# Kernel optimization log

Measured on AMD Instinct MI355X. Metric: run time of the kernel, lower is better.

The kernel has to match this reference:

```python
import jax, jax.numpy as jnp
import numpy as np

Q, N, S, A, E, H = 2048, 64, 128, 4, 128, 8
D = E // H
NEG = -1e9

def _mlp(x, w1, b1, w2, b2):
    return jax.nn.silu(x @ w1 + b1) @ w2 + b2

def _mha(x, wq, bq, wk, bk, wv, bv, wo, bo):
    # MultiHeadAttention with default activation=relu applied to q,k,v and output
    q = jax.nn.relu(x @ wq + bq)
    k = jax.nn.relu(x @ wk + bk)
    v = jax.nn.relu(x @ wv + bv)
    def split(t):
        return t.reshape(Q, N, H, D).transpose(0, 2, 1, 3)  # [Q,H,N,D]
    qh, kh, vh = split(q), split(k), split(v)
    scores = jnp.einsum('bhqd,bhkd->bhqk', qh, kh) / (D ** 0.5)
    attn = jax.nn.softmax(scores, axis=-1)
    y = jnp.einsum('bhqk,bhkd->bhqd', attn, vh).transpose(0, 2, 1, 3).reshape(Q, N, E)
    return jax.nn.relu(y @ wo + bo)

def setup_inputs():
    key = jax.random.key(0)
    ks = jax.random.split(key, 26)
    nrm = lambda k, s: jax.random.normal(k, s, jnp.float32) * 0.05
    return {
        'tasks': jax.random.normal(ks[0], (Q, N, N + 4 * S), jnp.float32),
        'constraints': jax.random.normal(ks[1], (Q, A), jnp.float32),
        'masks': jax.random.randint(ks[2], (Q, N, S), 0, 2),
        'topologicals': jax.random.randint(ks[3], (Q, N), 0, N),
        'w_init1': nrm(ks[4], (N + A, 128)), 'b_init1': jnp.zeros((128,), jnp.float32),
        'w_init2': nrm(ks[5], (128, E)), 'b_init2': jnp.zeros((E,), jnp.float32),
        'wq': nrm(ks[6], (E, E)), 'bq': jnp.zeros((E,), jnp.float32),
        'wk': nrm(ks[7], (E, E)), 'bk': jnp.zeros((E,), jnp.float32),
        'wv': nrm(ks[8], (E, E)), 'bv': jnp.zeros((E,), jnp.float32),
        'wo': nrm(ks[9], (E, E)), 'bo': jnp.zeros((E,), jnp.float32),
        'w_node1': nrm(ks[10], (E + A, 128)), 'b_node1': jnp.zeros((128,), jnp.float32),
        'w_node2': nrm(ks[11], (128, E)), 'b_node2': jnp.zeros((E,), jnp.float32),
        'w_ser1': nrm(ks[12], (A, 128)), 'b_ser1': jnp.zeros((128,), jnp.float32),
        'w_ser2': nrm(ks[13], (128, E)), 'b_ser2': jnp.zeros((E,), jnp.float32),
    }

def reference(tasks, constraints, masks, topologicals,
              w_init1, b_init1, w_init2, b_init2,
              wq, bq, wk, bk, wv, bv, wo, bo,
              w_node1, b_node1, w_node2, b_node2,
              w_ser1, b_ser1, w_ser2, b_ser2):
    cons = jnp.broadcast_to(constraints[:, None, :], (Q, N, A))
    node_emb = _mlp(jnp.concatenate([tasks[:, :, :N], cons], -1), w_init1, b_init1, w_init2, b_init2)
    nodes_emb = _mha(node_emb, wq, bq, wk, bk, wv, bv, wo, bo) + node_emb
    # original sets channel 0 to -3 then overwrites with 3; channel 2 stays 0 (kept faithfully)
    qos = jnp.zeros((Q, N, A), jnp.float32).at[:, :, 0].set(3.0).at[:, :, 1].set(1.0).at[:, :, 3].set(1.0)
    ava = jnp.ones((Q,), jnp.float32)
    tp = jnp.full((Q,), 3.0, jnp.float32)
    rel = jnp.ones((Q,), jnp.float32)
    ridx = jnp.zeros((Q, N), jnp.float32)
    rprob = jnp.zeros((Q, N), jnp.float32)
    qidx = jnp.arange(Q)
    topo_seq = topologicals[:, ::-1].T  # [N, Q]: reversed topological order, one node per step
    keys = jax.random.split(jax.random.key(1), N)

    def step(carry, xs):
        qos, ava, tp, rel, ridx, rprob = carry
        topo, k = xs
        task = tasks[qidx, topo]                 # [Q, N + 4S] per-query gathered row
        workflow = task[:, :N]
        response_time = jnp.max(workflow * qos[:, :, 0], axis=1)  # [Q]
        qos_feat = jnp.stack([response_time, ava, tp, rel], axis=-1)
        node_e = nodes_emb[qidx, topo]           # [Q, E]
        tne = _mlp(jnp.concatenate([node_e, qos_feat], -1), w_node1, b_node1, w_node2, b_node2)
        services = task[:, N:].reshape(Q, S, A)
        ser_emb = _mlp(services, w_ser1, b_ser1, w_ser2, b_ser2)
        logits = jnp.einsum('qse,qe->qs', ser_emb, tne)
        mask = masks[qidx, topo]                 # [Q, S]
        logits = jnp.where(mask == 0, NEG, logits)
        ser_prob = jax.nn.softmax(logits, axis=-1)
        ser_idx = jax.random.categorical(k, logits)  # ~ Categorical(ser_prob)
        onehot = jax.nn.one_hot(topo, N, dtype=jnp.float32)
        ridx = ridx + onehot * ser_idx[:, None].astype(jnp.float32)
        rprob = rprob + onehot * ser_prob[qidx, ser_idx][:, None]
        base = ser_idx * 4 + N
        ser_rt = task[qidx, base]
        ser_ava = task[qidx, base + 1]
        ser_tp = task[qidx, base + 2]
        ser_rel = task[qidx, base + 3]
        new_tp = jnp.minimum(ser_tp, tp)
        qos = qos.at[qidx, topo, 0].set(ser_rt + response_time)
        qos = qos.at[qidx, topo, 1].set(ser_ava * ava)
        qos = qos.at[qidx, topo, 2].set(new_tp)
        qos = qos.at[qidx, topo, 3].set(ser_rel * rel)
        return (qos, ser_ava * ava, new_tp, ser_rel * rel, ridx, rprob), None

    (qos, ava, tp, rel, ridx, rprob), _ = jax.lax.scan(
        step, (qos, ava, tp, rel, ridx, rprob), (topo_seq, keys))
    return ridx.astype(jnp.int16), rprob
```

## Files before the change

kernel.cpp:

```cpp
#include <hip/hip_runtime.h>
#include <math.h>

#define Qn 2048
#define Nn 64
#define Sn 128
#define An 4
#define En 128
#define TASKW 576
#define NEGV -1000000000.0f

__device__ __forceinline__ void threefry2x32(unsigned k0, unsigned k1,
                                             unsigned x0, unsigned x1,
                                             unsigned& o0, unsigned& o1) {
  unsigned ks2 = k0 ^ k1 ^ 0x1BD11BDAu;
  x0 += k0; x1 += k1;
#define TFR(r) { x0 += x1; x1 = (x1 << (r)) | (x1 >> (32 - (r))); x1 ^= x0; }
  TFR(13) TFR(15) TFR(26) TFR(6)
  x0 += k1;  x1 += ks2 + 1u;
  TFR(17) TFR(29) TFR(16) TFR(24)
  x0 += ks2; x1 += k0 + 2u;
  TFR(13) TFR(15) TFR(26) TFR(6)
  x0 += k0;  x1 += k1 + 3u;
  TFR(17) TFR(29) TFR(16) TFR(24)
  x0 += k1;  x1 += ks2 + 4u;
  TFR(13) TFR(15) TFR(26) TFR(6)
  x0 += ks2; x1 += k0 + 5u;
#undef TFR
  o0 = x0; o1 = x1;
}

__device__ __forceinline__ float silu_f(float x) {
  return x / (1.0f + expf(-x));
}

__device__ __forceinline__ float fexp(float x) {
  return __builtin_amdgcn_exp2f(x * 1.44269504088896f);
}
__device__ __forceinline__ float fsilu(float x) {
  const float e = __builtin_amdgcn_exp2f(x * -1.44269504088896f);
  return x * __builtin_amdgcn_rcpf(1.0f + e);
}
__device__ __forceinline__ float flog(float x) {
  return __builtin_amdgcn_logf(x) * 0.69314718055995f;
}

__global__ void setup_kernel(const float* __restrict__ w_node2,
                             const float* __restrict__ b_node2,
                             const float* __restrict__ w_ser2,
                             const float* __restrict__ b_ser2,
                             float* __restrict__ Mbuf, float* __restrict__ dvec,
                             unsigned* __restrict__ keys) {
  const int b = blockIdx.x, t = threadIdx.x;
  if (b < 128) {
    float acc = 0.0f;
    for (int e = 0; e < 128; ++e)
      acc = fmaf(w_node2[b * 128 + e], w_ser2[t * 128 + e], acc);
    Mbuf[b * 128 + t] = acc;
  } else if (b == 128) {
    float acc = 0.0f;
    for (int e = 0; e < 128; ++e)
      acc = fmaf(b_node2[e], w_ser2[t * 128 + e], acc);
    dvec[t] = acc;
  } else {
    if (t < 64) {
      unsigned o0, o1;
      threefry2x32(0u, 1u, 0u, (unsigned)t, o0, o1);
      keys[2 * t + 0] = o0;
      keys[2 * t + 1] = o1;
    }
  }
}

__global__ __launch_bounds__(256, 2)
void init_mlp_kernel(const float* __restrict__ tasks,
                     const float* __restrict__ cons,
                     const float* __restrict__ w1, const float* __restrict__ b1,
                     const float* __restrict__ w2, const float* __restrict__ b2,
                     float* __restrict__ node_emb) {
  const int q = blockIdx.x, tid = threadIdx.x;
  const int lane = tid & 127, half = tid >> 7;
  __shared__ float xr[2][68];
  __shared__ float sgb[2][128];
  float w1r[68], w2r[128];
#pragma unroll
  for (int i = 0; i < 68; ++i) w1r[i] = w1[i * 128 + lane];
#pragma unroll
  for (int j = 0; j < 128; ++j) w2r[j] = w2[j * 128 + lane];
  const float bb1 = b1[lane], bb2 = b2[lane];
  for (int r = 0; r < 64; r += 2) {
    if (tid < 136) {
      const int rr = tid / 68, j = tid - rr * 68;
      xr[rr][j] = (j < 64) ? tasks[(q * 64 + r + rr) * TASKW + j]
                           : cons[q * 4 + (j - 64)];
    }
    __syncthreads();
    float g = 0.0f;
#pragma unroll
    for (int i = 0; i < 68; ++i) g = fmaf(xr[half][i], w1r[i], g);
    g += bb1;
    sgb[half][lane] = silu_f(g);
    __syncthreads();
    float o = 0.0f;
#pragma unroll
    for (int j = 0; j < 128; ++j) o = fmaf(sgb[half][j], w2r[j], o);
    node_emb[(q * 64 + r + half) * 128 + lane] = o + bb2;
    __syncthreads();
  }
}

__global__ __launch_bounds__(256, 2)
void mha_kernel(const float* __restrict__ node_emb,
                const float* __restrict__ wq, const float* __restrict__ bq,
                const float* __restrict__ wk, const float* __restrict__ bk,
                const float* __restrict__ wv, const float* __restrict__ bv,
                float* __restrict__ y_out) {
  const int q = blockIdx.x, tid = threadIdx.x;
  __shared__ float xs[64][130];
  __shared__ float qh[64][18];
  __shared__ float kh[64][18];
  __shared__ float vt[16][66];
  __shared__ float pool[3 * 16 * 130];
  float (*wht)[16][130] = (float (*)[16][130])pool;
  float (*at)[66] = (float (*)[66])pool;

  for (int idx = tid; idx < 64 * 128; idx += 256) {
    const int n = idx >> 7, e = idx & 127;
    xs[n][e] = node_emb[(q * 64 + n) * 128 + e];
  }
  __syncthreads();

  const int d16 = tid >> 4;
  const int ng = tid & 15;

  for (int hd = 0; hd < 8; ++hd) {
    for (int idx = tid; idx < 3 * 128 * 16; idx += 256) {
      const int m = idx >> 11, k = (idx >> 4) & 127, d = idx & 15;
      const float* W = (m == 0) ? wq : (m == 1) ? wk : wv;
      wht[m][d][k] = W[k * 128 + hd * 16 + d];
    }
    __syncthreads();

    {
      const float bqv = bq[hd * 16 + d16];
      const float bkv = bk[hd * 16 + d16];
      const float bvv = bv[hd * 16 + d16];
      const float2* wq2 = (const float2*)&wht[0][d16][0];
      const float2* wk2 = (const float2*)&wht[1][d16][0];
      const float2* wv2 = (const float2*)&wht[2][d16][0];
      const float2* xr0 = (const float2*)&xs[ng][0];
      const float2* xr1 = (const float2*)&xs[ng + 16][0];
      const float2* xr2 = (const float2*)&xs[ng + 32][0];
      const float2* xr3 = (const float2*)&xs[ng + 48][0];
      float aq0 = 0, aq1 = 0, aq2 = 0, aq3 = 0;
      float ak0 = 0, ak1 = 0, ak2 = 0, ak3 = 0;
      float av0 = 0, av1 = 0, av2 = 0, av3 = 0;
#pragma unroll 8
      for (int kk = 0; kk < 64; ++kk) {
        const float2 wqv = wq2[kk], wkv = wk2[kk], wvv = wv2[kk];
        const float2 x0 = xr0[kk], x1 = xr1[kk], x2 = xr2[kk], x3 = xr3[kk];
        aq0 = fmaf(x0.y, wqv.y, fmaf(x0.x, wqv.x, aq0));
        aq1 = fmaf(x1.y, wqv.y, fmaf(x1.x, wqv.x, aq1));
        aq2 = fmaf(x2.y, wqv.y, fmaf(x2.x, wqv.x, aq2));
        aq3 = fmaf(x3.y, wqv.y, fmaf(x3.x, wqv.x, aq3));
        ak0 = fmaf(x0.y, wkv.y, fmaf(x0.x, wkv.x, ak0));
        ak1 = fmaf(x1.y, wkv.y, fmaf(x1.x, wkv.x, ak1));
        ak2 = fmaf(x2.y, wkv.y, fmaf(x2.x, wkv.x, ak2));
        ak3 = fmaf(x3.y, wkv.y, fmaf(x3.x, wkv.x, ak3));
        av0 = fmaf(x0.y, wvv.y, fmaf(x0.x, wvv.x, av0));
        av1 = fmaf(x1.y, wvv.y, fmaf(x1.x, wvv.x, av1));
        av2 = fmaf(x2.y, wvv.y, fmaf(x2.x, wvv.x, av2));
        av3 = fmaf(x3.y, wvv.y, fmaf(x3.x, wvv.x, av3));
      }
      qh[ng][d16] = fmaxf(aq0 + bqv, 0.0f);
      qh[ng + 16][d16] = fmaxf(aq1 + bqv, 0.0f);
      qh[ng + 32][d16] = fmaxf(aq2 + bqv, 0.0f);
      qh[ng + 48][d16] = fmaxf(aq3 + bqv, 0.0f);
      kh[ng][d16] = fmaxf(ak0 + bkv, 0.0f);
      kh[ng + 16][d16] = fmaxf(ak1 + bkv, 0.0f);
      kh[ng + 32][d16] = fmaxf(ak2 + bkv, 0.0f);
      kh[ng + 48][d16] = fmaxf(ak3 + bkv, 0.0f);
      vt[d16][ng] = fmaxf(av0 + bvv, 0.0f);
      vt[d16][ng + 16] = fmaxf(av1 + bvv, 0.0f);
      vt[d16][ng + 32] = fmaxf(av2 + bvv, 0.0f);
      vt[d16][ng + 48] = fmaxf(av3 + bvv, 0.0f);
    }
    __syncthreads();

    {
      const int n = tid >> 2, mg = tid & 3;
      float2 qv[8];
      const float2* qrow = (const float2*)&qh[n][0];
#pragma unroll
      for (int kk = 0; kk < 8; ++kk) qv[kk] = qrow[kk];
#pragma unroll 4
      for (int jj = 0; jj < 16; ++jj) {
        const int m = mg + 4 * jj;
        const float2* krow = (const float2*)&kh[m][0];
        float acc = 0.0f;
#pragma unroll
        for (int kk = 0; kk < 8; ++kk) {
          const float2 kv = krow[kk];
          acc = fmaf(qv[kk].y, kv.y, fmaf(qv[kk].x, kv.x, acc));
        }
        at[n][m] = acc * 0.25f;
      }
    }
    __syncthreads();

    {
      const int r = tid >> 2, p = tid & 3;
      float mx = -1e30f;
#pragma unroll
      for (int t2 = 0; t2 < 16; ++t2) mx = fmaxf(mx, at[r][p * 16 + t2]);
      mx = fmaxf(mx, __shfl_xor(mx, 1, 64));
      mx = fmaxf(mx, __shfl_xor(mx, 2, 64));
      float s = 0.0f;
#pragma unroll
      for (int t2 = 0; t2 < 16; ++t2) {
        const float e = fexp(at[r][p * 16 + t2] - mx);
        at[r][p * 16 + t2] = e;
        s += e;
      }
      s += __shfl_xor(s, 1, 64);
      s += __shfl_xor(s, 2, 64);
      const float rs = __builtin_amdgcn_rcpf(s);
#pragma unroll
      for (int t2 = 0; t2 < 16; ++t2) at[r][p * 16 + t2] *= rs;
    }
    __syncthreads();

    {
      const int dd = tid & 15, ngr = tid >> 4;
      const float2* vrow = (const float2*)&vt[dd][0];
      const float2* ar0 = (const float2*)&at[ngr][0];
      const float2* ar1 = (const float2*)&at[ngr + 16][0];
      const float2* ar2 = (const float2*)&at[ngr + 32][0];
      const float2* ar3 = (const float2*)&at[ngr + 48][0];
      float ac0 = 0, ac1 = 0, ac2 = 0, ac3 = 0;
#pragma unroll 8
      for (int kk = 0; kk < 32; ++kk) {
        const float2 vv = vrow[kk];
        const float2 a0 = ar0[kk], a1 = ar1[kk], a2 = ar2[kk], a3 = ar3[kk];
        ac0 = fmaf(a0.y, vv.y, fmaf(a0.x, vv.x, ac0));
        ac1 = fmaf(a1.y, vv.y, fmaf(a1.x, vv.x, ac1));
        ac2 = fmaf(a2.y, vv.y, fmaf(a2.x, vv.x, ac2));
        ac3 = fmaf(a3.y, vv.y, fmaf(a3.x, vv.x, ac3));
      }
      y_out[(q * 64 + ngr) * 128 + hd * 16 + dd] = ac0;
      y_out[(q * 64 + ngr + 16) * 128 + hd * 16 + dd] = ac1;
      y_out[(q * 64 + ngr + 32) * 128 + hd * 16 + dd] = ac2;
      y_out[(q * 64 + ngr + 48) * 128 + hd * 16 + dd] = ac3;
    }
    __syncthreads();
  }
}

__global__ __launch_bounds__(256, 4)
void outproj_kernel(const float* __restrict__ node_emb,
                    const float* __restrict__ wo, const float* __restrict__ bo,
                    float* __restrict__ nodes_emb) {
  const int q = blockIdx.x, tid = threadIdx.x;
  __shared__ float ys[64][130];
  __shared__ float wot[32][130];
  for (int idx = tid; idx < 64 * 128; idx += 256) {
    const int n = idx >> 7, e = idx & 127;
    ys[n][e] = nodes_emb[(q * 64 + n) * 128 + e];
  }
  const int cg = tid & 15, ngr = tid >> 4;
  for (int c0 = 0; c0 < 128; c0 += 32) {
    __syncthreads();
    for (int idx = tid; idx < 32 * 128; idx += 256) {
      const int k = idx >> 5, c = idx & 31;
      wot[c][k] = wo[k * 128 + c0 + c];
    }
    __syncthreads();
    const int c = c0 + 2 * cg;
    const float2* w0 = (const float2*)&wot[2 * cg][0];
    const float2* w1 = (const float2*)&wot[2 * cg + 1][0];
    const float2* yr0 = (const float2*)&ys[ngr][0];
    const float2* yr1 = (const float2*)&ys[ngr + 16][0];
    const float2* yr2 = (const float2*)&ys[ngr + 32][0];
    const float2* yr3 = (const float2*)&ys[ngr + 48][0];
    float a00 = 0, a01 = 0, a10 = 0, a11 = 0;
    float a20 = 0, a21 = 0, a30 = 0, a31 = 0;
#pragma unroll 8
    for (int kk = 0; kk < 64; ++kk) {
      const float2 wv0 = w0[kk], wv1 = w1[kk];
      const float2 x0 = yr0[kk], x1 = yr1[kk], x2 = yr2[kk], x3 = yr3[kk];
      a00 = fmaf(x0.y, wv0.y, fmaf(x0.x, wv0.x, a00));
      a01 = fmaf(x0.y, wv1.y, fmaf(x0.x, wv1.x, a01));
      a10 = fmaf(x1.y, wv0.y, fmaf(x1.x, wv0.x, a10));
      a11 = fmaf(x1.y, wv1.y, fmaf(x1.x, wv1.x, a11));
      a20 = fmaf(x2.y, wv0.y, fmaf(x2.x, wv0.x, a20));
      a21 = fmaf(x2.y, wv1.y, fmaf(x2.x, wv1.x, a21));
      a30 = fmaf(x3.y, wv0.y, fmaf(x3.x, wv0.x, a30));
      a31 = fmaf(x3.y, wv1.y, fmaf(x3.x, wv1.x, a31));
    }
    const float b0v = bo[c], b1v = bo[c + 1];
#define OUTP_EMIT(J, A0, A1)                                                  \
    {                                                                         \
      const int n = ngr + 16 * J;                                             \
      const float2 res = *(const float2*)&node_emb[(q * 64 + n) * 128 + c];   \
      float2 o;                                                               \
      o.x = fmaxf(A0 + b0v, 0.0f) + res.x;                                    \
      o.y = fmaxf(A1 + b1v, 0.0f) + res.y;                                    \
      *(float2*)&nodes_emb[(q * 64 + n) * 128 + c] = o;                       \
    }
    OUTP_EMIT(0, a00, a01)
    OUTP_EMIT(1, a10, a11)
    OUTP_EMIT(2, a20, a21)
    OUTP_EMIT(3, a30, a31)
#undef OUTP_EMIT
  }
}

__global__ __launch_bounds__(256, 4)
void gbase_kernel(const float* __restrict__ nodes_emb,
                  const float* __restrict__ w_node1,
                  const float* __restrict__ b_node1,
                  float* __restrict__ gbase) {
  const int q = blockIdx.x, tid = threadIdx.x;
  __shared__ float ys[64][130];
  __shared__ float wot[32][130];
  for (int idx = tid; idx < 64 * 128; idx += 256) {
    const int n = idx >> 7, e = idx & 127;
    ys[n][e] = nodes_emb[(q * 64 + n) * 128 + e];
  }
  const int cg = tid & 15, ngr = tid >> 4;
  for (int c0 = 0; c0 < 128; c0 += 32) {
    __syncthreads();
    for (int idx = tid; idx < 32 * 128; idx += 256) {
      const int k = idx >> 5, c = idx & 31;
      wot[c][k] = w_node1[k * 128 + c0 + c];
    }
    __syncthreads();
    const int c = c0 + 2 * cg;
    const float2* w0 = (const float2*)&wot[2 * cg][0];
    const float2* w1 = (const float2*)&wot[2 * cg + 1][0];
    const float2* yr0 = (const float2*)&ys[ngr][0];
    const float2* yr1 = (const float2*)&ys[ngr + 16][0];
    const float2* yr2 = (const float2*)&ys[ngr + 32][0];
    const float2* yr3 = (const float2*)&ys[ngr + 48][0];
    float a00 = 0, a01 = 0, a10 = 0, a11 = 0;
    float a20 = 0, a21 = 0, a30 = 0, a31 = 0;
#pragma unroll 8
    for (int kk = 0; kk < 64; ++kk) {
      const float2 wv0 = w0[kk], wv1 = w1[kk];
      const float2 x0 = yr0[kk], x1 = yr1[kk], x2 = yr2[kk], x3 = yr3[kk];
      a00 = fmaf(x0.y, wv0.y, fmaf(x0.x, wv0.x, a00));
      a01 = fmaf(x0.y, wv1.y, fmaf(x0.x, wv1.x, a01));
      a10 = fmaf(x1.y, wv0.y, fmaf(x1.x, wv0.x, a10));
      a11 = fmaf(x1.y, wv1.y, fmaf(x1.x, wv1.x, a11));
      a20 = fmaf(x2.y, wv0.y, fmaf(x2.x, wv0.x, a20));
      a21 = fmaf(x2.y, wv1.y, fmaf(x2.x, wv1.x, a21));
      a30 = fmaf(x3.y, wv0.y, fmaf(x3.x, wv0.x, a30));
      a31 = fmaf(x3.y, wv1.y, fmaf(x3.x, wv1.x, a31));
    }
    const float b0v = b_node1[c], b1v = b_node1[c + 1];
#define GB_EMIT(J, A0, A1)                                                    \
    {                                                                         \
      const int n = ngr + 16 * J;                                             \
      float2 o;                                                               \
      o.x = A0 + b0v;                                                         \
      o.y = A1 + b1v;                                                         \
      *(float2*)&gbase[(q * 64 + n) * 128 + c] = o;                           \
    }
    GB_EMIT(0, a00, a01)
    GB_EMIT(1, a10, a11)
    GB_EMIT(2, a20, a21)
    GB_EMIT(3, a30, a31)
#undef GB_EMIT
  }
}

__global__ __launch_bounds__(256, 4)
void scan_kernel(const float* __restrict__ tasks, const int* __restrict__ masks,
                 const int* __restrict__ topologicals,
                 const float* __restrict__ w_node1,
                 const float* __restrict__ w_ser1,
                 const float* __restrict__ b_ser1,
                 const float* __restrict__ gbase,
                 const float* __restrict__ Mbuf, const float* __restrict__ dvec,
                 const unsigned* __restrict__ keys, float* __restrict__ out) {
  const int q = blockIdx.x, tid = threadIdx.x;
  const int lane = tid & 127, half = tid >> 7;
  const int wl = tid & 63;

  __shared__ float task_s[2][TASKW];
  __shared__ float gb_s[2][128];
  __shared__ int mask_s[2][128];
  __shared__ int topo_s[64];
  __shared__ float sg[128];
  __shared__ float4 wst4[128];
  __shared__ float2 hp[128];
  __shared__ float logit_s[128];
  __shared__ float gl[128];
  __shared__ float red[256];
  __shared__ float qos_s[64 * 4];
  __shared__ float ridx_s[64], rprob_s[64];
  __shared__ float qw[4][128];
  __shared__ float dvs[128];
  __shared__ float scal[2];
  __shared__ int sidx_s;
  __shared__ unsigned keys_s[128];

  float Mr[64];
#pragma unroll
  for (int j = 0; j < 64; ++j) Mr[j] = Mbuf[(half * 64 + j) * 128 + lane];

  if (tid < 64) topo_s[tid] = topologicals[q * 64 + tid];
  if (tid < 128) {
    wst4[tid] = make_float4(w_ser1[tid], w_ser1[128 + tid], w_ser1[256 + tid],
                            w_ser1[384 + tid]);
    dvs[tid] = dvec[tid];
    keys_s[tid] = keys[tid];
  }
  for (int i = tid; i < 512; i += 256)
    qw[i >> 7][i & 127] = w_node1[(128 + (i >> 7)) * 128 + (i & 127)];
  if (tid < 64) {
    qos_s[tid * 4 + 0] = 3.0f;
    qos_s[tid * 4 + 1] = 1.0f;
    qos_s[tid * 4 + 2] = 0.0f;
    qos_s[tid * 4 + 3] = 1.0f;
    ridx_s[tid] = 0.0f;
    rprob_s[tid] = 0.0f;
  }
  const float bsl = b_ser1[lane];
  float ava = 1.0f, tp = 3.0f, rel = 1.0f;
  __syncthreads();

  {
    const int topo0 = topo_s[63];
    if (tid < 144)
      ((float4*)task_s[0])[tid] =
          ((const float4*)(tasks + (size_t)(q * 64 + topo0) * TASKW))[tid];
    if (tid < 128) {
      gb_s[0][tid] = gbase[(q * 64 + topo0) * 128 + tid];
      mask_s[0][tid] = masks[(q * 64 + topo0) * 128 + tid];
    }
  }
  __syncthreads();

  for (int t = 0; t < 64; ++t) {
    const int cur = t & 1, nxt = cur ^ 1;
    const int topo = topo_s[63 - t];

    float rt;
    {
      float p = task_s[cur][wl] * qos_s[wl * 4];
#pragma unroll
      for (int o = 32; o > 0; o >>= 1) p = fmaxf(p, __shfl_xor(p, o, 64));
      rt = p;
    }
    if (tid < 128) {
      float g = gb_s[cur][tid];
      g = fmaf(rt, qw[0][tid], g);
      g = fmaf(ava, qw[1][tid], g);
      g = fmaf(tp, qw[2][tid], g);
      g = fmaf(rel, qw[3][tid], g);
      sg[tid] = fsilu(g);
    }
    __syncthreads();

    {
      float acc = 0.0f;
      const float2* sg2 = (const float2*)sg + half * 32;
#pragma unroll
      for (int j = 0; j < 32; ++j) {
        const float2 x = sg2[j];
        acc = fmaf(x.x, Mr[2 * j], acc);
        acc = fmaf(x.y, Mr[2 * j + 1], acc);
      }
      red[tid] = acc;
    }
    __syncthreads();
    if (tid < 128) {
      const float uu = red[tid] + red[tid + 128] + dvs[tid];
      hp[tid] = make_float2(bsl, uu);
    }
    __syncthreads();

    float4 pf_task;
    float pf_gb;
    int pf_mask;
    {
      const int tn = (t < 63) ? t + 1 : 63;
      const int ntopo = topo_s[63 - tn];
      if (tid < 144)
        pf_task =
            ((const float4*)(tasks + (size_t)(q * 64 + ntopo) * TASKW))[tid];
      if (tid < 128) {
        pf_gb = gbase[(q * 64 + ntopo) * 128 + tid];
        pf_mask = masks[(q * 64 + ntopo) * 128 + tid];
      }
    }

    {
      const float4 sv = *(const float4*)&task_s[cur][64 + 4 * lane];
      float acc = 0.0f;
      const int hb = half * 64;
#pragma unroll 16
      for (int j = 0; j < 64; ++j) {
        const int h = hb + j;
        const float4 w = wst4[h];
        const float2 hb2 = hp[h];
        float h1 = fmaf(sv.x, w.x, hb2.x);
        h1 = fmaf(sv.y, w.y, h1);
        h1 = fmaf(sv.z, w.z, h1);
        h1 = fmaf(sv.w, w.w, h1);
        const float e = __builtin_amdgcn_exp2f(h1 * -1.44269504088896f);
        const float r = __builtin_amdgcn_rcpf(1.0f + e);
        acc = fmaf(h1 * r, hb2.y, acc);
      }
      red[tid] = acc;
    }
    __syncthreads();

    if (tid < 128) {
      float l = red[tid] + red[tid + 128];
      if (mask_s[cur][tid] == 0) l = NEGV;
      logit_s[tid] = l;
      unsigned o0, o1;
      threefry2x32(keys_s[2 * t], keys_s[2 * t + 1], 0u,
                   (unsigned)(q * 128 + tid), o0, o1);
      const unsigned bits = o0 ^ o1;
      const float f = __uint_as_float((bits >> 9) | 0x3f800000u) - 1.0f;
      const float u = (f > 0.0f) ? f : 1.17549435e-38f;
      const float gmb = -flog(-flog(u));
      gl[tid] = l + gmb;
    }
    if (tid < 144) ((float4*)task_s[nxt])[tid] = pf_task;
    if (tid < 128) {
      gb_s[nxt][tid] = pf_gb;
      mask_s[nxt][tid] = pf_mask;
    }
    __syncthreads();

    if (tid < 64) {
      float z = gl[tid];
      int zi = tid;
      const float z2 = gl[tid + 64];
      if (z2 > z) { z = z2; zi = tid + 64; }
#pragma unroll
      for (int o = 32; o > 0; o >>= 1) {
        const float zo = __shfl_xor(z, o, 64);
        const int io = __shfl_xor(zi, o, 64);
        if (zo > z || (zo == z && io < zi)) { z = zo; zi = io; }
      }
      if (tid == 0) sidx_s = zi;
    } else if (tid < 128) {
      const int l2 = tid - 64;
      const float la = logit_s[l2], lb = logit_s[l2 + 64];
      float mx = fmaxf(la, lb);
#pragma unroll
      for (int o = 32; o > 0; o >>= 1) mx = fmaxf(mx, __shfl_xor(mx, o, 64));
      float e = fexp(la - mx) + fexp(lb - mx);
#pragma unroll
      for (int o = 32; o > 0; o >>= 1) e += __shfl_xor(e, o, 64);
      if (l2 == 0) { scal[0] = mx; scal[1] = e; }
    }
    __syncthreads();

    {
      const int si = sidx_s;
      const float s1v = task_s[cur][64 + 4 * si + 1];
      const float s2v = task_s[cur][64 + 4 * si + 2];
      const float s3v = task_s[cur][64 + 4 * si + 3];
      if (tid == 0) {
        const float s0v = task_s[cur][64 + 4 * si];
        const float prob = fexp(logit_s[si] - scal[0]) / scal[1];
        qos_s[topo * 4 + 0] = s0v + rt;
        qos_s[topo * 4 + 1] = s1v * ava;
        qos_s[topo * 4 + 2] = fminf(s2v, tp);
        qos_s[topo * 4 + 3] = s3v * rel;
        ridx_s[topo] += (float)si;
        rprob_s[topo] += prob;
      }
      ava = s1v * ava;
      tp = fminf(s2v, tp);
      rel = s3v * rel;
    }
    __syncthreads();
  }
  if (tid < 64) {
    out[q * 64 + tid] = ridx_s[tid];
    out[Qn * Nn + q * 64 + tid] = rprob_s[tid];
  }
}

extern "C" void kernel_launch(void* const* d_in, const int* in_sizes, int n_in,
                              void* d_out, int out_size, void* d_ws,
                              size_t ws_size, hipStream_t stream) {
  const float* tasks = (const float*)d_in[0];
  const float* constraints = (const float*)d_in[1];
  const int* masks = (const int*)d_in[2];
  const int* topologicals = (const int*)d_in[3];
  const float* w_init1 = (const float*)d_in[4];
  const float* b_init1 = (const float*)d_in[5];
  const float* w_init2 = (const float*)d_in[6];
  const float* b_init2 = (const float*)d_in[7];
  const float* wq = (const float*)d_in[8];
  const float* bq = (const float*)d_in[9];
  const float* wk = (const float*)d_in[10];
  const float* bk = (const float*)d_in[11];
  const float* wv = (const float*)d_in[12];
  const float* bv = (const float*)d_in[13];
  const float* wo = (const float*)d_in[14];
  const float* bo = (const float*)d_in[15];
  const float* w_node1 = (const float*)d_in[16];
  const float* b_node1 = (const float*)d_in[17];
  const float* w_node2 = (const float*)d_in[18];
  const float* b_node2 = (const float*)d_in[19];
  const float* w_ser1 = (const float*)d_in[20];
  const float* b_ser1 = (const float*)d_in[21];
  const float* w_ser2 = (const float*)d_in[22];
  const float* b_ser2 = (const float*)d_in[23];

  float* ws = (float*)d_ws;
  float* node_emb = ws;
  float* nodes_emb = node_emb + (size_t)Qn * Nn * En;
  float* Mbuf = nodes_emb + (size_t)Qn * Nn * En;
  float* dvec = Mbuf + 128 * 128;
  unsigned* keys = (unsigned*)(dvec + 128);
  float* gbase = node_emb;

  setup_kernel<<<130, 128, 0, stream>>>(w_node2, b_node2, w_ser2, b_ser2, Mbuf,
                                        dvec, keys);
  init_mlp_kernel<<<Qn, 256, 0, stream>>>(tasks, constraints, w_init1, b_init1,
                                          w_init2, b_init2, node_emb);
  mha_kernel<<<Qn, 256, 0, stream>>>(node_emb, wq, bq, wk, bk, wv, bv,
                                     nodes_emb);
  outproj_kernel<<<Qn, 256, 0, stream>>>(node_emb, wo, bo, nodes_emb);
  gbase_kernel<<<Qn, 256, 0, stream>>>(nodes_emb, w_node1, b_node1, gbase);
  scan_kernel<<<Qn, 256, 0, stream>>>(tasks, masks, topologicals, w_node1,
                                      w_ser1, b_ser1, gbase, Mbuf, dvec, keys,
                                      (float*)d_out);
}
```

Measured before the change: 2.321 ms.

## Use packed FP32 FMA and compact logits to only unmasked services

```diff
diff --git a/kernel.cpp b/kernel.cpp
--- a/kernel.cpp
+++ b/kernel.cpp
@@ -8,6 +8,21 @@
 #define En 128
 #define TASKW 576
 #define NEGV -1000000000.0f
+
+typedef float v2f __attribute__((ext_vector_type(2)));
+
+__device__ __forceinline__ v2f mkv2(float a, float b) {
+  v2f r; r.x = a; r.y = b; return r;
+}
+__device__ __forceinline__ void pkfma(v2f& d, v2f a, v2f b) {
+  asm("v_pk_fma_f32 %0, %1, %2, %0" : "+v"(d) : "v"(a), "v"(b));
+}
+__device__ __forceinline__ v2f pkmul(v2f a, v2f b) {
+  v2f d; asm("v_pk_mul_f32 %0, %1, %2" : "=v"(d) : "v"(a), "v"(b)); return d;
+}
+__device__ __forceinline__ v2f pkadd(v2f a, v2f b) {
+  v2f d; asm("v_pk_add_f32 %0, %1, %2" : "=v"(d) : "v"(a), "v"(b)); return d;
+}
 
 __device__ __forceinline__ void threefry2x32(unsigned k0, unsigned k1,
                                              unsigned x0, unsigned x1,
@@ -79,13 +94,15 @@
                      float* __restrict__ node_emb) {
   const int q = blockIdx.x, tid = threadIdx.x;
   const int lane = tid & 127, half = tid >> 7;
-  __shared__ float xr[2][68];
-  __shared__ float sgb[2][128];
-  float w1r[68], w2r[128];
-#pragma unroll
-  for (int i = 0; i < 68; ++i) w1r[i] = w1[i * 128 + lane];
-#pragma unroll
-  for (int j = 0; j < 128; ++j) w2r[j] = w2[j * 128 + lane];
+  __shared__ __align__(16) float xr[2][68];
+  __shared__ __align__(16) float sgb[2][128];
+  v2f w1p[34], w2p[64];
+#pragma unroll
+  for (int i = 0; i < 34; ++i)
+    w1p[i] = mkv2(w1[(2 * i) * 128 + lane], w1[(2 * i + 1) * 128 + lane]);
+#pragma unroll
+  for (int j = 0; j < 64; ++j)
+    w2p[j] = mkv2(w2[(2 * j) * 128 + lane], w2[(2 * j + 1) * 128 + lane]);
   const float bb1 = b1[lane], bb2 = b2[lane];
   for (int r = 0; r < 64; r += 2) {
     if (tid < 136) {
@@ -94,16 +111,18 @@
                            : cons[q * 4 + (j - 64)];
     }
     __syncthreads();
-    float g = 0.0f;
-#pragma unroll
-    for (int i = 0; i < 68; ++i) g = fmaf(xr[half][i], w1r[i], g);
-    g += bb1;
+    v2f gp = mkv2(0.0f, 0.0f);
+    const v2f* xr2 = (const v2f*)&xr[half][0];
+#pragma unroll
+    for (int i = 0; i < 34; ++i) pkfma(gp, xr2[i], w1p[i]);
+    const float g = gp.x + gp.y + bb1;
     sgb[half][lane] = silu_f(g);
     __syncthreads();
-    float o = 0.0f;
-#pragma unroll
-    for (int j = 0; j < 128; ++j) o = fmaf(sgb[half][j], w2r[j], o);
-    node_emb[(q * 64 + r + half) * 128 + lane] = o + bb2;
+    v2f op = mkv2(0.0f, 0.0f);
+    const v2f* sgb2 = (const v2f*)&sgb[half][0];
+#pragma unroll
+    for (int j = 0; j < 64; ++j) pkfma(op, sgb2[j], w2p[j]);
+    node_emb[(q * 64 + r + half) * 128 + lane] = op.x + op.y + bb2;
     __syncthreads();
   }
 }
@@ -115,11 +134,11 @@
                 const float* __restrict__ wv, const float* __restrict__ bv,
                 float* __restrict__ y_out) {
   const int q = blockIdx.x, tid = threadIdx.x;
-  __shared__ float xs[64][130];
-  __shared__ float qh[64][18];
-  __shared__ float kh[64][18];
-  __shared__ float vt[16][66];
-  __shared__ float pool[3 * 16 * 130];
+  __shared__ __align__(16) float xs[64][130];
+  __shared__ __align__(16) float qh[64][18];
+  __shared__ __align__(16) float kh[64][18];
+  __shared__ __align__(16) float vt[16][66];
+  __shared__ __align__(16) float pool[3 * 16 * 130];
   float (*wht)[16][130] = (float (*)[16][130])pool;
   float (*at)[66] = (float (*)[66])pool;
 
@@ -144,65 +163,56 @@
       const float bqv = bq[hd * 16 + d16];
       const float bkv = bk[hd * 16 + d16];
       const float bvv = bv[hd * 16 + d16];
-      const float2* wq2 = (const float2*)&wht[0][d16][0];
-      const float2* wk2 = (const float2*)&wht[1][d16][0];
-      const float2* wv2 = (const float2*)&wht[2][d16][0];
-      const float2* xr0 = (const float2*)&xs[ng][0];
-      const float2* xr1 = (const float2*)&xs[ng + 16][0];
-      const float2* xr2 = (const float2*)&xs[ng + 32][0];
-      const float2* xr3 = (const float2*)&xs[ng + 48][0];
-      float aq0 = 0, aq1 = 0, aq2 = 0, aq3 = 0;
-      float ak0 = 0, ak1 = 0, ak2 = 0, ak3 = 0;
-      float av0 = 0, av1 = 0, av2 = 0, av3 = 0;
+      const v2f* wq2 = (const v2f*)&wht[0][d16][0];
+      const v2f* wk2 = (const v2f*)&wht[1][d16][0];
+      const v2f* wv2 = (const v2f*)&wht[2][d16][0];
+      const v2f* xr0 = (const v2f*)&xs[ng][0];
+      const v2f* xr1 = (const v2f*)&xs[ng + 16][0];
+      const v2f* xr2 = (const v2f*)&xs[ng + 32][0];
+      const v2f* xr3 = (const v2f*)&xs[ng + 48][0];
+      v2f aq0 = mkv2(0, 0), aq1 = mkv2(0, 0), aq2 = mkv2(0, 0), aq3 = mkv2(0, 0);
+      v2f ak0 = mkv2(0, 0), ak1 = mkv2(0, 0), ak2 = mkv2(0, 0), ak3 = mkv2(0, 0);
+      v2f av0 = mkv2(0, 0), av1 = mkv2(0, 0), av2 = mkv2(0, 0), av3 = mkv2(0, 0);
 #pragma unroll 8
       for (int kk = 0; kk < 64; ++kk) {
-        const float2 wqv = wq2[kk], wkv = wk2[kk], wvv = wv2[kk];
-        const float2 x0 = xr0[kk], x1 = xr1[kk], x2 = xr2[kk], x3 = xr3[kk];
-        aq0 = fmaf(x0.y, wqv.y, fmaf(x0.x, wqv.x, aq0));
-        aq1 = fmaf(x1.y, wqv.y, fmaf(x1.x, wqv.x, aq1));
-        aq2 = fmaf(x2.y, wqv.y, fmaf(x2.x, wqv.x, aq2));
-        aq3 = fmaf(x3.y, wqv.y, fmaf(x3.x, wqv.x, aq3));
-        ak0 = fmaf(x0.y, wkv.y, fmaf(x0.x, wkv.x, ak0));
-        ak1 = fmaf(x1.y, wkv.y, fmaf(x1.x, wkv.x, ak1));
-        ak2 = fmaf(x2.y, wkv.y, fmaf(x2.x, wkv.x, ak2));
-        ak3 = fmaf(x3.y, wkv.y, fmaf(x3.x, wkv.x, ak3));
-        av0 = fmaf(x0.y, wvv.y, fmaf(x0.x, wvv.x, av0));
-        av1 = fmaf(x1.y, wvv.y, fmaf(x1.x, wvv.x, av1));
-        av2 = fmaf(x2.y, wvv.y, fmaf(x2.x, wvv.x, av2));
-        av3 = fmaf(x3.y, wvv.y, fmaf(x3.x, wvv.x, av3));
-      }
-      qh[ng][d16] = fmaxf(aq0 + bqv, 0.0f);
-      qh[ng + 16][d16] = fmaxf(aq1 + bqv, 0.0f);
-      qh[ng + 32][d16] = fmaxf(aq2 + bqv, 0.0f);
-      qh[ng + 48][d16] = fmaxf(aq3 + bqv, 0.0f);
-      kh[ng][d16] = fmaxf(ak0 + bkv, 0.0f);
-      kh[ng + 16][d16] = fmaxf(ak1 + bkv, 0.0f);
-      kh[ng + 32][d16] = fmaxf(ak2 + bkv, 0.0f);
-      kh[ng + 48][d16] = fmaxf(ak3 + bkv, 0.0f);
-      vt[d16][ng] = fmaxf(av0 + bvv, 0.0f);
-      vt[d16][ng + 16] = fmaxf(av1 + bvv, 0.0f);
-      vt[d16][ng + 32] = fmaxf(av2 + bvv, 0.0f);
-      vt[d16][ng + 48] = fmaxf(av3 + bvv, 0.0f);
+        const v2f wqv = wq2[kk], wkv = wk2[kk], wvv = wv2[kk];
+        const v2f x0 = xr0[kk], x1 = xr1[kk], x2 = xr2[kk], x3 = xr3[kk];
+        pkfma(aq0, x0, wqv); pkfma(aq1, x1, wqv);
+        pkfma(aq2, x2, wqv); pkfma(aq3, x3, wqv);
+        pkfma(ak0, x0, wkv); pkfma(ak1, x1, wkv);
+        pkfma(ak2, x2, wkv); pkfma(ak3, x3, wkv);
+        pkfma(av0, x0, wvv); pkfma(av1, x1, wvv);
+        pkfma(av2, x2, wvv); pkfma(av3, x3, wvv);
+      }
+      qh[ng][d16] = fmaxf(aq0.x + aq0.y + bqv, 0.0f);
+      qh[ng + 16][d16] = fmaxf(aq1.x + aq1.y + bqv, 0.0f);
+      qh[ng + 32][d16] = fmaxf(aq2.x + aq2.y + bqv, 0.0f);
+      qh[ng + 48][d16] = fmaxf(aq3.x + aq3.y + bqv, 0.0f);
+      kh[ng][d16] = fmaxf(ak0.x + ak0.y + bkv, 0.0f);
+      kh[ng + 16][d16] = fmaxf(ak1.x + ak1.y + bkv, 0.0f);
+      kh[ng + 32][d16] = fmaxf(ak2.x + ak2.y + bkv, 0.0f);
+      kh[ng + 48][d16] = fmaxf(ak3.x + ak3.y + bkv, 0.0f);
+      vt[d16][ng] = fmaxf(av0.x + av0.y + bvv, 0.0f);
+      vt[d16][ng + 16] = fmaxf(av1.x + av1.y + bvv, 0.0f);
+      vt[d16][ng + 32] = fmaxf(av2.x + av2.y + bvv, 0.0f);
+      vt[d16][ng + 48] = fmaxf(av3.x + av3.y + bvv, 0.0f);
     }
     __syncthreads();
 
     {
       const int n = tid >> 2, mg = tid & 3;
-      float2 qv[8];
-      const float2* qrow = (const float2*)&qh[n][0];
+      v2f qv[8];
+      const v2f* qrow = (const v2f*)&qh[n][0];
 #pragma unroll
       for (int kk = 0; kk < 8; ++kk) qv[kk] = qrow[kk];
 #pragma unroll 4
       for (int jj = 0; jj < 16; ++jj) {
         const int m = mg + 4 * jj;
-        const float2* krow = (const float2*)&kh[m][0];
-        float acc = 0.0f;
-#pragma unroll
-        for (int kk = 0; kk < 8; ++kk) {
-          const float2 kv = krow[kk];
-          acc = fmaf(qv[kk].y, kv.y, fmaf(qv[kk].x, kv.x, acc));
-        }
-        at[n][m] = acc * 0.25f;
+        const v2f* krow = (const v2f*)&kh[m][0];
+        v2f accp = mkv2(0.0f, 0.0f);
+#pragma unroll
+        for (int kk = 0; kk < 8; ++kk) pkfma(accp, qv[kk], krow[kk]);
+        at[n][m] = (accp.x + accp.y) * 0.25f;
       }
     }
     __syncthreads();
@@ -231,25 +241,24 @@
 
     {
       const int dd = tid & 15, ngr = tid >> 4;
-      const float2* vrow = (const float2*)&vt[dd][0];
-      const float2* ar0 = (const float2*)&at[ngr][0];
-      const float2* ar1 = (const float2*)&at[ngr + 16][0];
-      const float2* ar2 = (const float2*)&at[ngr + 32][0];
-      const float2* ar3 = (const float2*)&at[ngr + 48][0];
-      float ac0 = 0, ac1 = 0, ac2 = 0, ac3 = 0;
+      const v2f* vrow = (const v2f*)&vt[dd][0];
+      const v2f* ar0 = (const v2f*)&at[ngr][0];
+      const v2f* ar1 = (const v2f*)&at[ngr + 16][0];
+      const v2f* ar2 = (const v2f*)&at[ngr + 32][0];
+      const v2f* ar3 = (const v2f*)&at[ngr + 48][0];
+      v2f ac0 = mkv2(0, 0), ac1 = mkv2(0, 0), ac2 = mkv2(0, 0), ac3 = mkv2(0, 0);
 #pragma unroll 8
       for (int kk = 0; kk < 32; ++kk) {
-        const float2 vv = vrow[kk];
-        const float2 a0 = ar0[kk], a1 = ar1[kk], a2 = ar2[kk], a3 = ar3[kk];
-        ac0 = fmaf(a0.y, vv.y, fmaf(a0.x, vv.x, ac0));
-        ac1 = fmaf(a1.y, vv.y, fmaf(a1.x, vv.x, ac1));
-        ac2 = fmaf(a2.y, vv.y, fmaf(a2.x, vv.x, ac2));
-        ac3 = fmaf(a3.y, vv.y, fmaf(a3.x, vv.x, ac3));
-      }
-      y_out[(q * 64 + ngr) * 128 + hd * 16 + dd] = ac0;
-      y_out[(q * 64 + ngr + 16) * 128 + hd * 16 + dd] = ac1;
-      y_out[(q * 64 + ngr + 32) * 128 + hd * 16 + dd] = ac2;
-      y_out[(q * 64 + ngr + 48) * 128 + hd * 16 + dd] = ac3;
+        const v2f vv = vrow[kk];
+        pkfma(ac0, ar0[kk], vv);
+        pkfma(ac1, ar1[kk], vv);
+        pkfma(ac2, ar2[kk], vv);
+        pkfma(ac3, ar3[kk], vv);
+      }
+      y_out[(q * 64 + ngr) * 128 + hd * 16 + dd] = ac0.x + ac0.y;
+      y_out[(q * 64 + ngr + 16) * 128 + hd * 16 + dd] = ac1.x + ac1.y;
+      y_out[(q * 64 + ngr + 32) * 128 + hd * 16 + dd] = ac2.x + ac2.y;
+      y_out[(q * 64 + ngr + 48) * 128 + hd * 16 + dd] = ac3.x + ac3.y;
     }
     __syncthreads();
   }
@@ -260,8 +269,8 @@
                     const float* __restrict__ wo, const float* __restrict__ bo,
                     float* __restrict__ nodes_emb) {
   const int q = blockIdx.x, tid = threadIdx.x;
-  __shared__ float ys[64][130];
-  __shared__ float wot[32][130];
+  __shared__ __align__(16) float ys[64][130];
+  __shared__ __align__(16) float wot[32][130];
   for (int idx = tid; idx < 64 * 128; idx += 256) {
     const int n = idx >> 7, e = idx & 127;
     ys[n][e] = nodes_emb[(q * 64 + n) * 128 + e];
@@ -275,26 +284,22 @@
     }
     __syncthreads();
     const int c = c0 + 2 * cg;
-    const float2* w0 = (const float2*)&wot[2 * cg][0];
-    const float2* w1 = (const float2*)&wot[2 * cg + 1][0];
-    const float2* yr0 = (const float2*)&ys[ngr][0];
-    const float2* yr1 = (const float2*)&ys[ngr + 16][0];
-    const float2* yr2 = (const float2*)&ys[ngr + 32][0];
-    const float2* yr3 = (const float2*)&ys[ngr + 48][0];
-    float a00 = 0, a01 = 0, a10 = 0, a11 = 0;
-    float a20 = 0, a21 = 0, a30 = 0, a31 = 0;
+    const v2f* w0 = (const v2f*)&wot[2 * cg][0];
+    const v2f* w1 = (const v2f*)&wot[2 * cg + 1][0];
+    const v2f* yr0 = (const v2f*)&ys[ngr][0];
+    const v2f* yr1 = (const v2f*)&ys[ngr + 16][0];
+    const v2f* yr2 = (const v2f*)&ys[ngr + 32][0];
+    const v2f* yr3 = (const v2f*)&ys[ngr + 48][0];
+    v2f a00 = mkv2(0, 0), a01 = mkv2(0, 0), a10 = mkv2(0, 0), a11 = mkv2(0, 0);
+    v2f a20 = mkv2(0, 0), a21 = mkv2(0, 0), a30 = mkv2(0, 0), a31 = mkv2(0, 0);
 #pragma unroll 8
     for (int kk = 0; kk < 64; ++kk) {
-      const float2 wv0 = w0[kk], wv1 = w1[kk];
-      const float2 x0 = yr0[kk], x1 = yr1[kk], x2 = yr2[kk], x3 = yr3[kk];
-      a00 = fmaf(x0.y, wv0.y, fmaf(x0.x, wv0.x, a00));
-      a01 = fmaf(x0.y, wv1.y, fmaf(x0.x, wv1.x, a01));
-      a10 = fmaf(x1.y, wv0.y, fmaf(x1.x, wv0.x, a10));
-      a11 = fmaf(x1.y, wv1.y, fmaf(x1.x, wv1.x, a11));
-      a20 = fmaf(x2.y, wv0.y, fmaf(x2.x, wv0.x, a20));
-      a21 = fmaf(x2.y, wv1.y, fmaf(x2.x, wv1.x, a21));
-      a30 = fmaf(x3.y, wv0.y, fmaf(x3.x, wv0.x, a30));
-      a31 = fmaf(x3.y, wv1.y, fmaf(x3.x, wv1.x, a31));
+      const v2f wv0 = w0[kk], wv1 = w1[kk];
+      const v2f x0 = yr0[kk], x1 = yr1[kk], x2 = yr2[kk], x3 = yr3[kk];
+      pkfma(a00, x0, wv0); pkfma(a01, x0, wv1);
+      pkfma(a10, x1, wv0); pkfma(a11, x1, wv1);
+      pkfma(a20, x2, wv0); pkfma(a21, x2, wv1);
+      pkfma(a30, x3, wv0); pkfma(a31, x3, wv1);
     }
     const float b0v = bo[c], b1v = bo[c + 1];
 #define OUTP_EMIT(J, A0, A1)                                                  \
@@ -302,8 +307,8 @@
       const int n = ngr + 16 * J;                                             \
       const float2 res = *(const float2*)&node_emb[(q * 64 + n) * 128 + c];   \
       float2 o;                                                               \
-      o.x = fmaxf(A0 + b0v, 0.0f) + res.x;                                    \
-      o.y = fmaxf(A1 + b1v, 0.0f) + res.y;                                    \
+      o.x = fmaxf(A0.x + A0.y + b0v, 0.0f) + res.x;                           \
+      o.y = fmaxf(A1.x + A1.y + b1v, 0.0f) + res.y;                           \
       *(float2*)&nodes_emb[(q * 64 + n) * 128 + c] = o;                       \
     }
     OUTP_EMIT(0, a00, a01)
@@ -320,8 +325,8 @@
                   const float* __restrict__ b_node1,
                   float* __restrict__ gbase) {
   const int q = blockIdx.x, tid = threadIdx.x;
-  __shared__ float ys[64][130];
-  __shared__ float wot[32][130];
+  __shared__ __align__(16) float ys[64][130];
+  __shared__ __align__(16) float wot[32][130];
   for (int idx = tid; idx < 64 * 128; idx += 256) {
     const int n = idx >> 7, e = idx & 127;
     ys[n][e] = nodes_emb[(q * 64 + n) * 128 + e];
@@ -335,34 +340,30 @@
     }
     __syncthreads();
     const int c = c0 + 2 * cg;
-    const float2* w0 = (const float2*)&wot[2 * cg][0];
-    const float2* w1 = (const float2*)&wot[2 * cg + 1][0];
-    const float2* yr0 = (const float2*)&ys[ngr][0];
-    const float2* yr1 = (const float2*)&ys[ngr + 16][0];
-    const float2* yr2 = (const float2*)&ys[ngr + 32][0];
-    const float2* yr3 = (const float2*)&ys[ngr + 48][0];
-    float a00 = 0, a01 = 0, a10 = 0, a11 = 0;
-    float a20 = 0, a21 = 0, a30 = 0, a31 = 0;
+    const v2f* w0 = (const v2f*)&wot[2 * cg][0];
+    const v2f* w1 = (const v2f*)&wot[2 * cg + 1][0];
+    const v2f* yr0 = (const v2f*)&ys[ngr][0];
+    const v2f* yr1 = (const v2f*)&ys[ngr + 16][0];
+    const v2f* yr2 = (const v2f*)&ys[ngr + 32][0];
+    const v2f* yr3 = (const v2f*)&ys[ngr + 48][0];
+    v2f a00 = mkv2(0, 0), a01 = mkv2(0, 0), a10 = mkv2(0, 0), a11 = mkv2(0, 0);
+    v2f a20 = mkv2(0, 0), a21 = mkv2(0, 0), a30 = mkv2(0, 0), a31 = mkv2(0, 0);
 #pragma unroll 8
     for (int kk = 0; kk < 64; ++kk) {
-      const float2 wv0 = w0[kk], wv1 = w1[kk];
-      const float2 x0 = yr0[kk], x1 = yr1[kk], x2 = yr2[kk], x3 = yr3[kk];
-      a00 = fmaf(x0.y, wv0.y, fmaf(x0.x, wv0.x, a00));
-      a01 = fmaf(x0.y, wv1.y, fmaf(x0.x, wv1.x, a01));
-      a10 = fmaf(x1.y, wv0.y, fmaf(x1.x, wv0.x, a10));
-      a11 = fmaf(x1.y, wv1.y, fmaf(x1.x, wv1.x, a11));
-      a20 = fmaf(x2.y, wv0.y, fmaf(x2.x, wv0.x, a20));
-      a21 = fmaf(x2.y, wv1.y, fmaf(x2.x, wv1.x, a21));
-      a30 = fmaf(x3.y, wv0.y, fmaf(x3.x, wv0.x, a30));
-      a31 = fmaf(x3.y, wv1.y, fmaf(x3.x, wv1.x, a31));
+      const v2f wv0 = w0[kk], wv1 = w1[kk];
+      const v2f x0 = yr0[kk], x1 = yr1[kk], x2 = yr2[kk], x3 = yr3[kk];
+      pkfma(a00, x0, wv0); pkfma(a01, x0, wv1);
+      pkfma(a10, x1, wv0); pkfma(a11, x1, wv1);
+      pkfma(a20, x2, wv0); pkfma(a21, x2, wv1);
+      pkfma(a30, x3, wv0); pkfma(a31, x3, wv1);
     }
     const float b0v = b_node1[c], b1v = b_node1[c + 1];
 #define GB_EMIT(J, A0, A1)                                                    \
     {                                                                         \
       const int n = ngr + 16 * J;                                             \
       float2 o;                                                               \
-      o.x = A0 + b0v;                                                         \
-      o.y = A1 + b1v;                                                         \
+      o.x = A0.x + A0.y + b0v;                                                \
+      o.y = A1.x + A1.y + b1v;                                                \
       *(float2*)&gbase[(q * 64 + n) * 128 + c] = o;                           \
     }
     GB_EMIT(0, a00, a01)
@@ -385,33 +386,44 @@
   const int q = blockIdx.x, tid = threadIdx.x;
   const int lane = tid & 127, half = tid >> 7;
   const int wl = tid & 63;
-
-  __shared__ float task_s[2][TASKW];
-  __shared__ float gb_s[2][128];
+  const int wave = tid >> 6;
+
+  __shared__ __align__(16) float task_s[2][TASKW];
+  __shared__ __align__(16) float gb_s[2][128];
   __shared__ int mask_s[2][128];
   __shared__ int topo_s[64];
-  __shared__ float sg[128];
-  __shared__ float4 wst4[128];
-  __shared__ float2 hp[128];
-  __shared__ float logit_s[128];
-  __shared__ float gl[128];
-  __shared__ float red[256];
+  __shared__ __align__(16) float sg[128];
+  __shared__ __align__(16) v2f warr_s[64][4];
+  __shared__ __align__(16) v2f bp_s[64];
+  __shared__ __align__(16) v2f up_s[64];
+  __shared__ __align__(16) float red[256];
+  __shared__ float lcomp_s[128];
+  __shared__ float gla_s[128];
+  __shared__ int act_s[128];
   __shared__ float qos_s[64 * 4];
   __shared__ float ridx_s[64], rprob_s[64];
-  __shared__ float qw[4][128];
-  __shared__ float dvs[128];
+  __shared__ __align__(16) float qw[4][128];
+  __shared__ __align__(16) float dvs[128];
   __shared__ float scal[2];
-  __shared__ int sidx_s;
+  __shared__ int sidx_s, kstar_s, na_s;
   __shared__ unsigned keys_s[128];
 
-  float Mr[64];
-#pragma unroll
-  for (int j = 0; j < 64; ++j) Mr[j] = Mbuf[(half * 64 + j) * 128 + lane];
-
-  if (tid < 64) topo_s[tid] = topologicals[q * 64 + tid];
+  v2f Mr2[32];
+#pragma unroll
+  for (int j = 0; j < 32; ++j)
+    Mr2[j] = mkv2(Mbuf[(half * 64 + 2 * j) * 128 + lane],
+                  Mbuf[(half * 64 + 2 * j + 1) * 128 + lane]);
+
+  if (tid < 64) {
+    topo_s[tid] = topologicals[q * 64 + tid];
+    const int j = tid, sl = ((j & 15) << 2) | (j >> 4);
+#pragma unroll
+    for (int c = 0; c < 4; ++c)
+      warr_s[sl][c] =
+          mkv2(w_ser1[c * 128 + 2 * j], w_ser1[c * 128 + 2 * j + 1]);
+    bp_s[sl] = mkv2(b_ser1[2 * j], b_ser1[2 * j + 1]);
+  }
   if (tid < 128) {
-    wst4[tid] = make_float4(w_ser1[tid], w_ser1[128 + tid], w_ser1[256 + tid],
-                            w_ser1[384 + tid]);
     dvs[tid] = dvec[tid];
     keys_s[tid] = keys[tid];
   }
@@ -425,7 +437,6 @@
     ridx_s[tid] = 0.0f;
     rprob_s[tid] = 0.0f;
   }
-  const float bsl = b_ser1[lane];
   float ava = 1.0f, tp = 3.0f, rel = 1.0f;
   __syncthreads();
 
@@ -445,12 +456,22 @@
     const int cur = t & 1, nxt = cur ^ 1;
     const int topo = topo_s[63 - t];
 
-    float rt;
-    {
+    float rt = 0.0f;
+    if (wave < 2) {
       float p = task_s[cur][wl] * qos_s[wl * 4];
 #pragma unroll
       for (int o = 32; o > 0; o >>= 1) p = fmaxf(p, __shfl_xor(p, o, 64));
       rt = p;
+    } else if (wave == 2) {
+      const int m0 = mask_s[cur][wl] != 0;
+      const int m1 = mask_s[cur][wl + 64] != 0;
+      const unsigned long long b0 = __ballot(m0);
+      const unsigned long long b1 = __ballot(m1);
+      const unsigned long long lt = (1ull << wl) - 1ull;
+      const int c0 = __popcll(b0);
+      if (m0) act_s[__popcll(b0 & lt)] = wl;
+      if (m1) act_s[c0 + __popcll(b1 & lt)] = wl + 64;
+      if (wl == 0) na_s = c0 + __popcll(b1);
     }
     if (tid < 128) {
       float g = gb_s[cur][tid];
@@ -463,20 +484,18 @@
     __syncthreads();
 
     {
-      float acc = 0.0f;
-      const float2* sg2 = (const float2*)sg + half * 32;
-#pragma unroll
-      for (int j = 0; j < 32; ++j) {
-        const float2 x = sg2[j];
-        acc = fmaf(x.x, Mr[2 * j], acc);
-        acc = fmaf(x.y, Mr[2 * j + 1], acc);
-      }
-      red[tid] = acc;
-    }
-    __syncthreads();
-    if (tid < 128) {
-      const float uu = red[tid] + red[tid + 128] + dvs[tid];
-      hp[tid] = make_float2(bsl, uu);
+      v2f accp = mkv2(0.0f, 0.0f);
+      const v2f* sg2 = (const v2f*)sg + half * 32;
+#pragma unroll
+      for (int j = 0; j < 32; ++j) pkfma(accp, sg2[j], Mr2[j]);
+      red[tid] = accp.x + accp.y;
+    }
+    __syncthreads();
+    if (tid < 64) {
+      const v2f r0 = *(const v2f*)&red[2 * tid];
+      const v2f r1 = *(const v2f*)&red[2 * tid + 128];
+      const v2f dv = *(const v2f*)&dvs[2 * tid];
+      up_s[((tid & 15) << 2) | (tid >> 4)] = pkadd(pkadd(r0, r1), dv);
     }
     __syncthreads();
 
@@ -495,39 +514,62 @@
       }
     }
 
-    {
-      const float4 sv = *(const float4*)&task_s[cur][64 + 4 * lane];
-      float acc = 0.0f;
-      const int hb = half * 64;
-#pragma unroll 16
-      for (int j = 0; j < 64; ++j) {
-        const int h = hb + j;
-        const float4 w = wst4[h];
-        const float2 hb2 = hp[h];
-        float h1 = fmaf(sv.x, w.x, hb2.x);
-        h1 = fmaf(sv.y, w.y, h1);
-        h1 = fmaf(sv.z, w.z, h1);
-        h1 = fmaf(sv.w, w.w, h1);
-        const float e = __builtin_amdgcn_exp2f(h1 * -1.44269504088896f);
-        const float r = __builtin_amdgcn_rcpf(1.0f + e);
-        acc = fmaf(h1 * r, hb2.y, acc);
-      }
-      red[tid] = acc;
+    const int na = na_s;
+    {
+      const int si = tid >> 2, hq = tid & 3;
+      float ls[2];
+#pragma unroll
+      for (int rep = 0; rep < 2; ++rep) {
+        const int slot = si + 64 * rep;
+        float lv = 0.0f;
+        if (slot < na) {
+          const int s = act_s[slot];
+          const float4 sv = *(const float4*)&task_s[cur][64 + 4 * s];
+          const v2f svx = mkv2(sv.x, sv.x), svy = mkv2(sv.y, sv.y);
+          const v2f svz = mkv2(sv.z, sv.z), svw = mkv2(sv.w, sv.w);
+          v2f acc = mkv2(0.0f, 0.0f);
+#pragma unroll
+          for (int jj = 0; jj < 16; ++jj) {
+            const int sl = (jj << 2) | hq;
+            v2f p = bp_s[sl];
+            pkfma(p, svx, warr_s[sl][0]);
+            pkfma(p, svy, warr_s[sl][1]);
+            pkfma(p, svz, warr_s[sl][2]);
+            pkfma(p, svw, warr_s[sl][3]);
+            const v2f e =
+                pkmul(p, mkv2(-1.44269504088896f, -1.44269504088896f));
+            const float ex = __builtin_amdgcn_exp2f(e.x);
+            const float ey = __builtin_amdgcn_exp2f(e.y);
+            const float rx = __builtin_amdgcn_rcpf(1.0f + ex);
+            const float ry = __builtin_amdgcn_rcpf(1.0f + ey);
+            pkfma(acc, mkv2(p.x * rx, p.y * ry), up_s[sl]);
+          }
+          lv = acc.x + acc.y;
+        }
+        lv += __shfl_xor(lv, 1, 64);
+        lv += __shfl_xor(lv, 2, 64);
+        ls[rep] = lv;
+      }
+      if (hq == 0) {
+        if (si < na) lcomp_s[si] = ls[0];
+        if (si + 64 < na) lcomp_s[si + 64] = ls[1];
+      }
     }
     __syncthreads();
 
     if (tid < 128) {
-      float l = red[tid] + red[tid + 128];
-      if (mask_s[cur][tid] == 0) l = NEGV;
-      logit_s[tid] = l;
-      unsigned o0, o1;
-      threefry2x32(keys_s[2 * t], keys_s[2 * t + 1], 0u,
-                   (unsigned)(q * 128 + tid), o0, o1);
-      const unsigned bits = o0 ^ o1;
-      const float f = __uint_as_float((bits >> 9) | 0x3f800000u) - 1.0f;
-      const float u = (f > 0.0f) ? f : 1.17549435e-38f;
-      const float gmb = -flog(-flog(u));
-      gl[tid] = l + gmb;
+      float gv = -3.0e38f;
+      if (tid < na) {
+        const int s = act_s[tid];
+        unsigned o0, o1;
+        threefry2x32(keys_s[2 * t], keys_s[2 * t + 1], 0u,
+                     (unsigned)(q * 128 + s), o0, o1);
+        const unsigned bits = o0 ^ o1;
+        const float f = __uint_as_float((bits >> 9) | 0x3f800000u) - 1.0f;
+        const float u = (f > 0.0f) ? f : 1.17549435e-38f;
+        gv = lcomp_s[tid] - flog(-flog(u));
+      }
+      gla_s[tid] = gv;
     }
     if (tid < 144) ((float4*)task_s[nxt])[tid] = pf_task;
     if (tid < 128) {
@@ -537,9 +579,9 @@
     __syncthreads();
 
     if (tid < 64) {
-      float z = gl[tid];
+      float z = gla_s[tid];
       int zi = tid;
-      const float z2 = gl[tid + 64];
+      const float z2 = gla_s[tid + 64];
       if (z2 > z) { z = z2; zi = tid + 64; }
 #pragma unroll
       for (int o = 32; o > 0; o >>= 1) {
@@ -547,10 +589,14 @@
         const int io = __shfl_xor(zi, o, 64);
         if (zo > z || (zo == z && io < zi)) { z = zo; zi = io; }
       }
-      if (tid == 0) sidx_s = zi;
+      if (tid == 0) {
+        kstar_s = zi;
+        sidx_s = act_s[zi];
+      }
     } else if (tid < 128) {
       const int l2 = tid - 64;
-      const float la = logit_s[l2], lb = logit_s[l2 + 64];
+      const float la = (l2 < na) ? lcomp_s[l2] : -3.0e38f;
+      const float lb = (l2 + 64 < na) ? lcomp_s[l2 + 64] : -3.0e38f;
       float mx = fmaxf(la, lb);
 #pragma unroll
       for (int o = 32; o > 0; o >>= 1) mx = fmaxf(mx, __shfl_xor(mx, o, 64));
@@ -568,7 +614,7 @@
       const float s3v = task_s[cur][64 + 4 * si + 3];
       if (tid == 0) {
         const float s0v = task_s[cur][64 + 4 * si];
-        const float prob = fexp(logit_s[si] - scal[0]) / scal[1];
+        const float prob = fexp(lcomp_s[kstar_s] - scal[0]) / scal[1];
         qos_s[topo * 4 + 0] = s0v + rt;
         qos_s[topo * 4 + 1] = s1v * ava;
         qos_s[topo * 4 + 2] = fminf(s2v, tp);
```

New measurement: 2.226 ms. -4.1%, faster.
